# Kernel tuning notes

Hardware: AMD Instinct MI355X
Metric: run time of the kernel (lower is better)

Reference implementation:

```python
import jax, jax.numpy as jnp
import numpy as np

D = 64        # in_out_dim
M = 512       # hidden_dim
N = 4096      # batch
R = 10        # rank of quadratic term A (min(10, d+1))
ALPHA0 = 1.0  # alpha[0]
H = 1.0       # ResNet step h = 1/(nTh-1), nTh=2


def antideriv_tanh(x):
    # log(2*cosh(x)), numerically stable antiderivative of tanh
    ax = jnp.abs(x)
    return ax + jnp.log1p(jnp.exp(-2.0 * ax))


def setup_inputs() -> dict:
    key = jax.random.key(0)
    ks = jax.random.split(key, 10)
    f32 = jnp.float32
    return {
        "x":   jax.random.normal(ks[0], (N, D), f32),
        "t":   jax.random.uniform(ks[1], (), f32),
        "K0":  jax.random.normal(ks[2], (M, D + 1), f32) * (1.0 / np.sqrt(D + 1)),
        "b0":  jax.random.normal(ks[3], (M,), f32) * 0.1,
        "K1":  jax.random.normal(ks[4], (M, M), f32) * (1.0 / np.sqrt(M)),
        "b1":  jax.random.normal(ks[5], (M,), f32) * 0.1,
        "w":   jax.random.normal(ks[6], (M,), f32) * (1.0 / np.sqrt(M)),
        "A":   jax.random.normal(ks[7], (R, D + 1), f32) * (1.0 / np.sqrt(D + 1)),
        "c_w": jax.random.normal(ks[8], (D + 1,), f32) * 0.1,
        "c_b": jax.random.normal(ks[9], (), f32) * 0.1,
    }


def _tr_hess(s, K0, b0, K1, b1, w, A, c_w):
    # s: [N, d+1]; analytic gradient + Hessian trace of the OT-Flow potential.
    d = s.shape[1] - 1
    symA = A.T @ A                                   # [d+1, d+1]

    # forward through ResNet (nTh=2 -> one residual layer)
    opening = s @ K0.T + b0                          # [N, m]
    u0 = antideriv_tanh(opening)                     # [N, m]
    lin1 = u0 @ K1.T + b1                            # [N, m]

    tanh_open = jnp.tanh(opening)
    tanh_lin1 = jnp.tanh(lin1)

    # backward z-chain for the gradient
    z1 = w + H * (tanh_lin1 * w) @ K1                # [N, m]
    z0 = (tanh_open * z1) @ K0                       # [N, d+1]
    grad = z0 + s @ symA + c_w                       # [N, d+1]

    # trace of Hessian w.r.t. the first d coordinates
    Kopen = K0[:, :d]                                # [m, d]
    dt_open = 1.0 - tanh_open ** 2
    trH = (dt_open * z1) @ jnp.sum(Kopen ** 2, axis=1)          # [N]
    Jac = tanh_open[:, :, None] * Kopen[None]                    # [N, m, d]
    KJ = jnp.einsum('ij,njk->nik', K1, Jac)                      # [N, m, d]
    dt_lin1 = 1.0 - tanh_lin1 ** 2
    t1 = jnp.einsum('nj,njk->n', dt_lin1 * w, KJ ** 2)           # [N]
    trH = trH + H * t1 + jnp.trace(symA[:d, :d])
    return grad, trH


def reference(x, t, K0, b0, K1, b1, w, A, c_w, c_b):
    n = x.shape[0]
    s = jnp.concatenate([x, jnp.ones((n, 1), x.dtype) * t], axis=1)  # pad time
    gradPhi, trH = _tr_hess(s, K0, b0, K1, b1, w, A, c_w)
    dPhi_dx = gradPhi[:, :D]                         # [N, d]
    dPhi_dt = gradPhi[:, D:D + 1]                    # [N, 1]
    dz_dt = -(1.0 / ALPHA0) * dPhi_dx
    dlogp_dt = -(1.0 / ALPHA0) * trH[:, None]
    cost_L_dt = 0.5 * jnp.sum(dz_dt ** 2, axis=1, keepdims=True)
    cost_HJB_dt = jnp.abs(-dPhi_dt + ALPHA0 * cost_L_dt)
    return (dz_dt, dlogp_dt, cost_L_dt, cost_HJB_dt)
```

## Files before the change

### kernel.cpp

```cpp
#include <hip/hip_runtime.h>
#include <stdint.h>

#define D_  64
#define DP1 65
#define M_  512
#define N_  4096

typedef float f32x4 __attribute__((ext_vector_type(4)));
typedef _Float16 h8 __attribute__((ext_vector_type(8)));

__global__ void prep1(const float* __restrict__ A, const float* __restrict__ K0,
                      float* symA, float* sumK2, float* params){
  int t = threadIdx.x;
  for (int idx = t; idx < DP1*DP1; idx += 256){
    int e = idx / DP1, d = idx % DP1;
    float s = 0.f;
    for (int r = 0; r < 10; ++r) s += A[r*DP1+e]*A[r*DP1+d];
    symA[idx] = s;
  }
  for (int m = t; m < M_; m += 256){
    float s = 0.f;
    for (int k = 0; k < D_; ++k){ float v = K0[m*DP1+k]; s += v*v; }
    sumK2[m] = s;
  }
  __syncthreads();
  if (t == 0){
    float tr = 0.f;
    for (int d = 0; d < D_; ++d) tr += symA[d*DP1+d];
    params[0] = tr;
  }
}

__global__ void prep2(const float* __restrict__ K1, _Float16* K1h, _Float16* K1Th){
  __shared__ float tile[64][65];
  int r0 = blockIdx.x*64, c0 = blockIdx.y*64;
  int t = threadIdx.x;
  for (int it = 0; it < 16; ++it){
    int lin = it*256 + t;
    int r = lin >> 6, c = lin & 63;
    float v = K1[(r0+r)*M_ + c0+c];
    tile[r][c] = v;
    K1h[(r0+r)*M_ + c0+c] = (_Float16)v;
  }
  __syncthreads();
  for (int it = 0; it < 16; ++it){
    int lin = it*256 + t;
    int r = lin >> 6, c = lin & 63;
    K1Th[(c0+r)*M_ + (r0+c)] = (_Float16)tile[c][r];
  }
}

__global__ void prep3(const float* __restrict__ K0, _Float16* K0Th){
  int idx = blockIdx.x*256 + threadIdx.x;
  if (idx >= 80*M_) return;
  int d = idx / M_, i = idx % M_;
  float v = (d < DP1) ? K0[i*DP1 + d] : 0.f;
  K0Th[idx] = (_Float16)v;
}

__global__ void openk(const float* __restrict__ x, const float* __restrict__ tptr,
                      const float* __restrict__ K0, const float* __restrict__ b0,
                      _Float16* u0h, _Float16* ah,
                      float* trH0, const float* __restrict__ params){
  __shared__ float sS[64][66];
  __shared__ float sK[64][66];
  int n0 = blockIdx.x*64, m0 = blockIdx.y*64;
  int t = threadIdx.x;
  float tval = tptr[0];
  for (int it = 0; it < 17; ++it){
    int lin = it*256 + t;
    if (lin < 64*65){
      int r = lin/65, c = lin%65;
      sS[r][c] = (c < 64) ? x[(n0+r)*64 + c] : tval;
      sK[r][c] = K0[(m0+r)*DP1 + c];
    }
  }
  __syncthreads();
  int tn = (t>>4)*4, tm = (t&15)*4;
  float acc[4][4] = {};
  for (int e = 0; e < DP1; ++e){
    float sv[4], kv[4];
    for (int i=0;i<4;++i){ sv[i]=sS[tn+i][e]; kv[i]=sK[tm+i][e]; }
    for (int i=0;i<4;++i) for(int j=0;j<4;++j) acc[i][j] += sv[i]*kv[j];
  }
  for (int i=0;i<4;++i) for(int j=0;j<4;++j){
    int n = n0+tn+i, m = m0+tm+j;
    float o = acc[i][j] + b0[m];
    float a = tanhf(o);
    float ax = fabsf(o);
    float u0 = ax + log1pf(expf(-2.f*ax));
    u0h[n*M_+m] = (_Float16)u0;
    ah[n*M_+m]  = (_Float16)a;
  }
  if (m0 == 0 && t < 64) trH0[n0+t] = params[0];
}

template<int MODE>
__launch_bounds__(256, 4)
__global__ void gemm512(const _Float16* __restrict__ Ah, const _Float16* __restrict__ Wh,
                        const float* __restrict__ bias, const float* __restrict__ w,
                        const _Float16* __restrict__ ah, const float* __restrict__ sumK2,
                        _Float16* out0, _Float16* out1, float* trH0){
  int n0 = blockIdx.x*64, i0 = blockIdx.y*64;
  int t = threadIdx.x;
  int wv = t>>6, l = t&63;
  int r15 = l & 15;
  int krow = (l>>4)*8;
  const _Float16* abase = Ah + (size_t)(n0 + wv*16 + r15)*M_ + krow;
  const _Float16* wb0 = Wh + (size_t)(i0 +  0 + r15)*M_ + krow;
  const _Float16* wb1 = Wh + (size_t)(i0 + 16 + r15)*M_ + krow;
  const _Float16* wb2 = Wh + (size_t)(i0 + 32 + r15)*M_ + krow;
  const _Float16* wb3 = Wh + (size_t)(i0 + 48 + r15)*M_ + krow;
  f32x4 zero = {0.f,0.f,0.f,0.f};
  f32x4 acc[4]; for (int k=0;k<4;++k) acc[k]=zero;
  h8 af_c = *(const h8*)(abase);
  h8 bf_c0 = *(const h8*)(wb0);
  h8 bf_c1 = *(const h8*)(wb1);
  h8 bf_c2 = *(const h8*)(wb2);
  h8 bf_c3 = *(const h8*)(wb3);
  #pragma unroll
  for (int ii = 0; ii < 16; ++ii){
    const int j0 = ii*32;
    h8 af_n, bf_n0, bf_n1, bf_n2, bf_n3;
    if (ii < 15){
      af_n  = *(const h8*)(abase + j0 + 32);
      bf_n0 = *(const h8*)(wb0 + j0 + 32);
      bf_n1 = *(const h8*)(wb1 + j0 + 32);
      bf_n2 = *(const h8*)(wb2 + j0 + 32);
      bf_n3 = *(const h8*)(wb3 + j0 + 32);
    }
    acc[0] = __builtin_amdgcn_mfma_f32_16x16x32_f16(af_c, bf_c0, acc[0], 0, 0, 0);
    acc[1] = __builtin_amdgcn_mfma_f32_16x16x32_f16(af_c, bf_c1, acc[1], 0, 0, 0);
    acc[2] = __builtin_amdgcn_mfma_f32_16x16x32_f16(af_c, bf_c2, acc[2], 0, 0, 0);
    acc[3] = __builtin_amdgcn_mfma_f32_16x16x32_f16(af_c, bf_c3, acc[3], 0, 0, 0);
    if (ii < 15){
      af_c = af_n; bf_c0 = bf_n0; bf_c1 = bf_n1; bf_c2 = bf_n2; bf_c3 = bf_n3;
    }
  }
  if (MODE == 0){
    for (int kt=0;kt<4;++kt) for (int r=0;r<4;++r){
      int n = n0+wv*16+(l>>4)*4+r;
      int i = i0+kt*16+r15;
      float v = acc[kt][r] + bias[i];
      float tl = tanhf(v);
      out0[n*M_+i] = (_Float16)(tl*w[i]);
      out1[n*M_+i] = (_Float16)((1.f-tl*tl)*w[i]);
    }
  } else {
    for (int r=0;r<4;++r){
      int n = n0+wv*16+(l>>4)*4+r;
      float rowpart = 0.f;
      for (int kt=0;kt<4;++kt){
        int i = i0+kt*16+r15;
        float z1 = acc[kt][r] + w[i];
        float a = (float)ah[n*M_+i];
        out0[n*M_+i] = (_Float16)(a*z1);
        rowpart += (1.f-a*a)*z1*sumK2[i];
      }
      for (int m=1;m<16;m<<=1) rowpart += __shfl_xor(rowpart, m);
      if (r15==0) atomicAdd(&trH0[n], rowpart);
    }
  }
}

__launch_bounds__(256, 4)
__global__ void gemmz0(const _Float16* __restrict__ az1h, const _Float16* __restrict__ K0Th,
                       float* z0){
  int n0 = blockIdx.x*64;
  int t = threadIdx.x, wv = t>>6, l = t&63;
  int r15 = l & 15;
  int krow = (l>>4)*8;
  const _Float16* abase = az1h + (size_t)(n0 + wv*16 + r15)*M_ + krow;
  const _Float16* kb0 = K0Th + (size_t)( 0 + r15)*M_ + krow;
  const _Float16* kb1 = K0Th + (size_t)(16 + r15)*M_ + krow;
  const _Float16* kb2 = K0Th + (size_t)(32 + r15)*M_ + krow;
  const _Float16* kb3 = K0Th + (size_t)(48 + r15)*M_ + krow;
  const _Float16* kb4 = K0Th + (size_t)(64 + r15)*M_ + krow;
  f32x4 zero = {0.f,0.f,0.f,0.f};
  f32x4 acc[5]; for (int k=0;k<5;++k) acc[k]=zero;
  h8 af_c = *(const h8*)(abase);
  h8 b0c = *(const h8*)(kb0);
  h8 b1c = *(const h8*)(kb1);
  h8 b2c = *(const h8*)(kb2);
  h8 b3c = *(const h8*)(kb3);
  h8 b4c = *(const h8*)(kb4);
  #pragma unroll
  for (int ii = 0; ii < 16; ++ii){
    const int j0 = ii*32;
    h8 af_n, b0n, b1n, b2n, b3n, b4n;
    if (ii < 15){
      af_n = *(const h8*)(abase + j0 + 32);
      b0n = *(const h8*)(kb0 + j0 + 32);
      b1n = *(const h8*)(kb1 + j0 + 32);
      b2n = *(const h8*)(kb2 + j0 + 32);
      b3n = *(const h8*)(kb3 + j0 + 32);
      b4n = *(const h8*)(kb4 + j0 + 32);
    }
    acc[0] = __builtin_amdgcn_mfma_f32_16x16x32_f16(af_c, b0c, acc[0], 0, 0, 0);
    acc[1] = __builtin_amdgcn_mfma_f32_16x16x32_f16(af_c, b1c, acc[1], 0, 0, 0);
    acc[2] = __builtin_amdgcn_mfma_f32_16x16x32_f16(af_c, b2c, acc[2], 0, 0, 0);
    acc[3] = __builtin_amdgcn_mfma_f32_16x16x32_f16(af_c, b3c, acc[3], 0, 0, 0);
    acc[4] = __builtin_amdgcn_mfma_f32_16x16x32_f16(af_c, b4c, acc[4], 0, 0, 0);
    if (ii < 15){
      af_c = af_n; b0c = b0n; b1c = b1n; b2c = b2n; b3c = b3n; b4c = b4n;
    }
  }
  for (int dt=0; dt<5; ++dt) for (int r=0;r<4;++r){
    int n = n0+wv*16+(l>>4)*4+r;
    int d = dt*16+r15;
    z0[n*80+d] = acc[dt][r];
  }
}

__launch_bounds__(256, 2)
__global__ void kjk9(const _Float16* __restrict__ K1h, const _Float16* __restrict__ K0Th,
                     const _Float16* __restrict__ ah, const _Float16* __restrict__ ch,
                     float* trH0){
  __shared__ _Float16 sK1[64*512];
  __shared__ _Float16 sAv[8*512];
  int t = threadIdx.x;
  int n0 = blockIdx.x*8;
  int i0 = blockIdx.y*64;
  int wv = t>>6, l = t&63;
  int c15 = l & 15, g = l>>4;
  h8 kf[16];
  {
    const _Float16* kfp = K0Th + (size_t)(wv*16 + c15)*M_ + g*8;
    #pragma unroll
    for (int tt = 0; tt < 16; ++tt) kf[tt] = *(const h8*)(kfp + tt*32);
  }
  #pragma unroll
  for (int it = 0; it < 16; ++it){
    int cc = it*256 + t;
    int r = cc >> 6, c = cc & 63;
    h8 v = *(const h8*)(K1h + (size_t)(i0 + r)*M_ + c*8);
    *(h8*)(&sK1[r*512 + ((c ^ (r & 7))*8)]) = v;
  }
  #pragma unroll
  for (int it = 0; it < 2; ++it){
    int cc = it*256 + t;
    int s = cc >> 6, c = cc & 63;
    *(h8*)(&sAv[s*512 + c*8]) = *(const h8*)(ah + (size_t)(n0+s)*M_ + c*8);
  }
  __syncthreads();
  f32x4 zero = {0.f,0.f,0.f,0.f};
  f32x4 acc[4][8];
  #pragma unroll
  for (int tt=0;tt<4;++tt)
    #pragma unroll
    for (int s=0;s<8;++s) acc[tt][s]=zero;
  #pragma unroll
  for (int step = 0; step < 16; ++step){
    int p0 = (((step*4 + g) ^ (c15 & 7))*8);
    h8 bf0 = *(const h8*)(&sK1[(     c15)*512 + p0]);
    h8 bf1 = *(const h8*)(&sK1[(16 + c15)*512 + p0]);
    h8 bf2 = *(const h8*)(&sK1[(32 + c15)*512 + p0]);
    h8 bf3 = *(const h8*)(&sK1[(48 + c15)*512 + p0]);
    int aoff = step*32 + g*8;
    h8 k = kf[step];
    #pragma unroll
    for (int s = 0; s < 8; ++s){
      h8 av = *(const h8*)(&sAv[s*512 + aoff]);
      h8 ap = k*av;
      acc[0][s] = __builtin_amdgcn_mfma_f32_16x16x32_f16(ap, bf0, acc[0][s], 0, 0, 0);
      acc[1][s] = __builtin_amdgcn_mfma_f32_16x16x32_f16(ap, bf1, acc[1][s], 0, 0, 0);
      acc[2][s] = __builtin_amdgcn_mfma_f32_16x16x32_f16(ap, bf2, acc[2][s], 0, 0, 0);
      acc[3][s] = __builtin_amdgcn_mfma_f32_16x16x32_f16(ap, bf3, acc[3][s], 0, 0, 0);
    }
  }
  #pragma unroll
  for (int s = 0; s < 8; ++s){
    float part = 0.f;
    #pragma unroll
    for (int tt = 0; tt < 4; ++tt){
      float ci = (float)ch[(size_t)(n0+s)*M_ + i0 + tt*16 + c15];
      f32x4 a = acc[tt][s];
      part += ci*(a[0]*a[0] + a[1]*a[1] + a[2]*a[2] + a[3]*a[3]);
    }
    for (int m=32;m>=1;m>>=1) part += __shfl_xor(part, m);
    if (l == 0) atomicAdd(&trH0[n0+s], part);
  }
}

__global__ void finalk(const float* __restrict__ x, const float* __restrict__ tptr,
                       const float* __restrict__ symA, const float* __restrict__ c_w,
                       const float* __restrict__ z0, const float* __restrict__ trH0,
                       float* out){
  __shared__ float sA[DP1*DP1];
  int t = threadIdx.x;
  for (int i = t; i < DP1*DP1; i += 256) sA[i] = symA[i];
  __syncthreads();
  int wv = t>>6, l = t&63;
  int n = blockIdx.x*4 + wv;
  float tval = tptr[0];
  float sv = x[n*64 + l];
  float acc = z0[n*80 + l] + c_w[l];
  for (int e = 0; e < 64; ++e){
    float se = __shfl(sv, e);
    acc += se * sA[l*DP1 + e];
  }
  acc += tval * sA[l*DP1 + 64];
  float g64 = sv * sA[64*DP1 + l];
  for (int m=32;m>=1;m>>=1) g64 += __shfl_xor(g64, m);
  g64 += tval*sA[64*DP1+64] + z0[n*80+64] + c_w[64];
  float dz = -acc;
  out[n*64 + l] = dz;
  float q = dz*dz;
  for (int m=32;m>=1;m>>=1) q += __shfl_xor(q, m);
  float costL = 0.5f*q;
  if (l == 0){
    out[N_*64 + n]        = -trH0[n];
    out[N_*64 + N_ + n]   = costL;
    out[N_*64 + 2*N_ + n] = fabsf(-g64 + costL);
  }
}

extern "C" void kernel_launch(void* const* d_in, const int* in_sizes, int n_in,
                              void* d_out, int out_size, void* d_ws, size_t ws_size,
                              hipStream_t stream){
  const float* x   = (const float*)d_in[0];
  const float* tp  = (const float*)d_in[1];
  const float* K0  = (const float*)d_in[2];
  const float* b0  = (const float*)d_in[3];
  const float* K1  = (const float*)d_in[4];
  const float* b1  = (const float*)d_in[5];
  const float* w   = (const float*)d_in[6];
  const float* A   = (const float*)d_in[7];
  const float* c_w = (const float*)d_in[8];
  float* out = (float*)d_out;

  char* ws = (char*)d_ws;
  size_t off = 0;
  auto alloc = [&](size_t bytes)->void*{
    void* p = ws + off; off += bytes; off = (off + 255) & ~(size_t)255; return p;
  };
  _Float16* K1h   = (_Float16*)alloc(512*512*2);
  _Float16* K1Th  = (_Float16*)alloc(512*512*2);
  _Float16* K0Th  = (_Float16*)alloc(80*512*2);
  float* symA     = (float*)alloc(DP1*DP1*4);
  float* sumK2    = (float*)alloc(512*4);
  float* params   = (float*)alloc(256);
  _Float16* u0h   = (_Float16*)alloc((size_t)N_*M_*2);
  _Float16* ah    = (_Float16*)alloc((size_t)N_*M_*2);
  _Float16* tl1wh = (_Float16*)alloc((size_t)N_*M_*2);
  _Float16* ch    = (_Float16*)alloc((size_t)N_*M_*2);
  _Float16* az1h  = (_Float16*)alloc((size_t)N_*M_*2);
  float* z0       = (float*)alloc((size_t)N_*80*4);
  float* trH0     = (float*)alloc(N_*4);

  prep1<<<1, 256, 0, stream>>>(A, K0, symA, sumK2, params);
  prep2<<<dim3(8,8), 256, 0, stream>>>(K1, K1h, K1Th);
  prep3<<<160, 256, 0, stream>>>(K0, K0Th);
  openk<<<dim3(N_/64, M_/64), 256, 0, stream>>>(x, tp, K0, b0, u0h, ah, trH0, params);
  gemm512<0><<<dim3(N_/64, M_/64), 256, 0, stream>>>(u0h, K1h, b1, w, nullptr, nullptr,
                                                     tl1wh, ch, nullptr);
  gemm512<1><<<dim3(N_/64, M_/64), 256, 0, stream>>>(tl1wh, K1Th, nullptr, w, ah, sumK2,
                                                     az1h, nullptr, trH0);
  gemmz0<<<N_/64, 256, 0, stream>>>(az1h, K0Th, z0);
  kjk9<<<dim3(N_/8, 8), 256, 0, stream>>>(K1h, K0Th, ah, ch, trH0);
  finalk<<<N_/4, 256, 0, stream>>>(x, tp, symA, c_w, z0, trH0, out);
}
```

Measured before the change: 235.2 us.

## Merge prep and opening kernels, load K1 tile via global_load_lds in kjk

Four small preprocessing kernels and the opening-layer kernel are merged into a single launch whose block index selects the role. This removes three launch boundaries and serialization gaps. The symA trace term moves into the final kernel as a wave reduction, so trH0 is simply zeroed. In the Hessian-trace kernel, the K1 tile is staged into LDS with direct global-to-LDS loads, and the activation rows are read straight from global memory instead of through LDS, trading LDS traffic for repeated global/L1 loads.

```diff
diff --git a/kernel.cpp b/kernel.cpp
--- a/kernel.cpp
+++ b/kernel.cpp
@@ -9,90 +9,84 @@
 typedef float f32x4 __attribute__((ext_vector_type(4)));
 typedef _Float16 h8 __attribute__((ext_vector_type(8)));
 
-__global__ void prep1(const float* __restrict__ A, const float* __restrict__ K0,
-                      float* symA, float* sumK2, float* params){
+__global__ void prepk(const float* __restrict__ A, const float* __restrict__ K0,
+                      const float* __restrict__ K1, const float* __restrict__ x,
+                      const float* __restrict__ tptr, const float* __restrict__ b0,
+                      float* symA, float* sumK2,
+                      _Float16* K1h, _Float16* K1Th, _Float16* K0Th,
+                      _Float16* u0h, _Float16* ah, float* trH0){
+  __shared__ float shm[2*64*66];
+  int b = blockIdx.x;
   int t = threadIdx.x;
-  for (int idx = t; idx < DP1*DP1; idx += 256){
-    int e = idx / DP1, d = idx % DP1;
-    float s = 0.f;
-    for (int r = 0; r < 10; ++r) s += A[r*DP1+e]*A[r*DP1+d];
-    symA[idx] = s;
-  }
-  for (int m = t; m < M_; m += 256){
-    float s = 0.f;
-    for (int k = 0; k < D_; ++k){ float v = K0[m*DP1+k]; s += v*v; }
-    sumK2[m] = s;
-  }
-  __syncthreads();
-  if (t == 0){
-    float tr = 0.f;
-    for (int d = 0; d < D_; ++d) tr += symA[d*DP1+d];
-    params[0] = tr;
-  }
-}
-
-__global__ void prep2(const float* __restrict__ K1, _Float16* K1h, _Float16* K1Th){
-  __shared__ float tile[64][65];
-  int r0 = blockIdx.x*64, c0 = blockIdx.y*64;
-  int t = threadIdx.x;
-  for (int it = 0; it < 16; ++it){
-    int lin = it*256 + t;
-    int r = lin >> 6, c = lin & 63;
-    float v = K1[(r0+r)*M_ + c0+c];
-    tile[r][c] = v;
-    K1h[(r0+r)*M_ + c0+c] = (_Float16)v;
-  }
-  __syncthreads();
-  for (int it = 0; it < 16; ++it){
-    int lin = it*256 + t;
-    int r = lin >> 6, c = lin & 63;
-    K1Th[(c0+r)*M_ + (r0+c)] = (_Float16)tile[c][r];
-  }
-}
-
-__global__ void prep3(const float* __restrict__ K0, _Float16* K0Th){
-  int idx = blockIdx.x*256 + threadIdx.x;
-  if (idx >= 80*M_) return;
-  int d = idx / M_, i = idx % M_;
-  float v = (d < DP1) ? K0[i*DP1 + d] : 0.f;
-  K0Th[idx] = (_Float16)v;
-}
-
-__global__ void openk(const float* __restrict__ x, const float* __restrict__ tptr,
-                      const float* __restrict__ K0, const float* __restrict__ b0,
-                      _Float16* u0h, _Float16* ah,
-                      float* trH0, const float* __restrict__ params){
-  __shared__ float sS[64][66];
-  __shared__ float sK[64][66];
-  int n0 = blockIdx.x*64, m0 = blockIdx.y*64;
-  int t = threadIdx.x;
-  float tval = tptr[0];
-  for (int it = 0; it < 17; ++it){
-    int lin = it*256 + t;
-    if (lin < 64*65){
-      int r = lin/65, c = lin%65;
-      sS[r][c] = (c < 64) ? x[(n0+r)*64 + c] : tval;
-      sK[r][c] = K0[(m0+r)*DP1 + c];
-    }
-  }
-  __syncthreads();
-  int tn = (t>>4)*4, tm = (t&15)*4;
-  float acc[4][4] = {};
-  for (int e = 0; e < DP1; ++e){
-    float sv[4], kv[4];
-    for (int i=0;i<4;++i){ sv[i]=sS[tn+i][e]; kv[i]=sK[tm+i][e]; }
-    for (int i=0;i<4;++i) for(int j=0;j<4;++j) acc[i][j] += sv[i]*kv[j];
-  }
-  for (int i=0;i<4;++i) for(int j=0;j<4;++j){
-    int n = n0+tn+i, m = m0+tm+j;
-    float o = acc[i][j] + b0[m];
-    float a = tanhf(o);
-    float ax = fabsf(o);
-    float u0 = ax + log1pf(expf(-2.f*ax));
-    u0h[n*M_+m] = (_Float16)u0;
-    ah[n*M_+m]  = (_Float16)a;
-  }
-  if (m0 == 0 && t < 64) trH0[n0+t] = params[0];
+  if (b == 0){
+    for (int idx = t; idx < DP1*DP1; idx += 256){
+      int e = idx / DP1, d = idx % DP1;
+      float s = 0.f;
+      for (int r = 0; r < 10; ++r) s += A[r*DP1+e]*A[r*DP1+d];
+      symA[idx] = s;
+    }
+    for (int m = t; m < M_; m += 256){
+      float s = 0.f;
+      for (int k = 0; k < D_; ++k){ float v = K0[m*DP1+k]; s += v*v; }
+      sumK2[m] = s;
+    }
+  } else if (b < 65){
+    int bb = b - 1;
+    int r0 = (bb>>3)*64, c0 = (bb&7)*64;
+    float* tile = shm;
+    for (int it = 0; it < 16; ++it){
+      int lin = it*256 + t;
+      int r = lin >> 6, c = lin & 63;
+      float v = K1[(r0+r)*M_ + c0+c];
+      tile[r*65+c] = v;
+      K1h[(r0+r)*M_ + c0+c] = (_Float16)v;
+    }
+    __syncthreads();
+    for (int it = 0; it < 16; ++it){
+      int lin = it*256 + t;
+      int r = lin >> 6, c = lin & 63;
+      K1Th[(c0+r)*M_ + (r0+c)] = (_Float16)tile[c*65+r];
+    }
+  } else if (b < 225){
+    int idx = (b-65)*256 + t;
+    if (idx < 80*M_){
+      int d = idx / M_, i = idx % M_;
+      float v = (d < DP1) ? K0[i*DP1 + d] : 0.f;
+      K0Th[idx] = (_Float16)v;
+    }
+  } else {
+    int bb = b - 225;
+    int n0 = (bb & 63)*64, m0 = (bb >> 6)*64;
+    float* sS = shm;
+    float* sK = shm + 64*66;
+    float tval = tptr[0];
+    for (int it = 0; it < 17; ++it){
+      int lin = it*256 + t;
+      if (lin < 64*65){
+        int r = lin/65, c = lin%65;
+        sS[r*66+c] = (c < 64) ? x[(n0+r)*64 + c] : tval;
+        sK[r*66+c] = K0[(m0+r)*DP1 + c];
+      }
+    }
+    __syncthreads();
+    int tn = (t>>4)*4, tm = (t&15)*4;
+    float acc[4][4] = {};
+    for (int e = 0; e < DP1; ++e){
+      float sv[4], kv[4];
+      for (int i=0;i<4;++i){ sv[i]=sS[(tn+i)*66+e]; kv[i]=sK[(tm+i)*66+e]; }
+      for (int i=0;i<4;++i) for(int j=0;j<4;++j) acc[i][j] += sv[i]*kv[j];
+    }
+    for (int i=0;i<4;++i) for(int j=0;j<4;++j){
+      int n = n0+tn+i, m = m0+tm+j;
+      float o = acc[i][j] + b0[m];
+      float a = tanhf(o);
+      float ax = fabsf(o);
+      float u0 = ax + log1pf(expf(-2.f*ax));
+      u0h[n*M_+m] = (_Float16)u0;
+      ah[n*M_+m]  = (_Float16)a;
+    }
+    if (m0 == 0 && t < 64) trH0[n0+t] = 0.f;
+  }
 }
 
 template<int MODE>
@@ -213,11 +207,10 @@
 }
 
 __launch_bounds__(256, 2)
-__global__ void kjk9(const _Float16* __restrict__ K1h, const _Float16* __restrict__ K0Th,
-                     const _Float16* __restrict__ ah, const _Float16* __restrict__ ch,
-                     float* trH0){
+__global__ void kjk10(const _Float16* __restrict__ K1h, const _Float16* __restrict__ K0Th,
+                      const _Float16* __restrict__ ah, const _Float16* __restrict__ ch,
+                      float* trH0){
   __shared__ _Float16 sK1[64*512];
-  __shared__ _Float16 sAv[8*512];
   int t = threadIdx.x;
   int n0 = blockIdx.x*8;
   int i0 = blockIdx.y*64;
@@ -231,16 +224,11 @@
   }
   #pragma unroll
   for (int it = 0; it < 16; ++it){
-    int cc = it*256 + t;
-    int r = cc >> 6, c = cc & 63;
-    h8 v = *(const h8*)(K1h + (size_t)(i0 + r)*M_ + c*8);
-    *(h8*)(&sK1[r*512 + ((c ^ (r & 7))*8)]) = v;
-  }
-  #pragma unroll
-  for (int it = 0; it < 2; ++it){
-    int cc = it*256 + t;
-    int s = cc >> 6, c = cc & 63;
-    *(h8*)(&sAv[s*512 + c*8]) = *(const h8*)(ah + (size_t)(n0+s)*M_ + c*8);
+    int r = it*4 + wv;
+    const _Float16* src = K1h + (size_t)(i0 + r)*M_ + ((l ^ (r & 7))*8);
+    __builtin_amdgcn_global_load_lds(
+        (const __attribute__((address_space(1))) void*)src,
+        (__attribute__((address_space(3))) void*)(&sK1[r*512]), 16, 0, 0);
   }
   __syncthreads();
   f32x4 zero = {0.f,0.f,0.f,0.f};
@@ -249,6 +237,7 @@
   for (int tt=0;tt<4;++tt)
     #pragma unroll
     for (int s=0;s<8;++s) acc[tt][s]=zero;
+  const _Float16* ab = ah + (size_t)n0*M_ + g*8;
   #pragma unroll
   for (int step = 0; step < 16; ++step){
     int p0 = (((step*4 + g) ^ (c15 & 7))*8);
@@ -256,11 +245,10 @@
     h8 bf1 = *(const h8*)(&sK1[(16 + c15)*512 + p0]);
     h8 bf2 = *(const h8*)(&sK1[(32 + c15)*512 + p0]);
     h8 bf3 = *(const h8*)(&sK1[(48 + c15)*512 + p0]);
-    int aoff = step*32 + g*8;
     h8 k = kf[step];
     #pragma unroll
     for (int s = 0; s < 8; ++s){
-      h8 av = *(const h8*)(&sAv[s*512 + aoff]);
+      h8 av = *(const h8*)(ab + (size_t)s*M_ + step*32);
       h8 ap = k*av;
       acc[0][s] = __builtin_amdgcn_mfma_f32_16x16x32_f16(ap, bf0, acc[0][s], 0, 0, 0);
       acc[1][s] = __builtin_amdgcn_mfma_f32_16x16x32_f16(ap, bf1, acc[1][s], 0, 0, 0);
@@ -300,6 +288,8 @@
     acc += se * sA[l*DP1 + e];
   }
   acc += tval * sA[l*DP1 + 64];
+  float trd = sA[l*66];
+  for (int m=32;m>=1;m>>=1) trd += __shfl_xor(trd, m);
   float g64 = sv * sA[64*DP1 + l];
   for (int m=32;m>=1;m>>=1) g64 += __shfl_xor(g64, m);
   g64 += tval*sA[64*DP1+64] + z0[n*80+64] + c_w[64];
@@ -309,7 +299,7 @@
   for (int m=32;m>=1;m>>=1) q += __shfl_xor(q, m);
   float costL = 0.5f*q;
   if (l == 0){
-    out[N_*64 + n]        = -trH0[n];
+    out[N_*64 + n]        = -(trH0[n] + trd);
     out[N_*64 + N_ + n]   = costL;
     out[N_*64 + 2*N_ + n] = fabsf(-g64 + costL);
   }
@@ -339,7 +329,6 @@
   _Float16* K0Th  = (_Float16*)alloc(80*512*2);
   float* symA     = (float*)alloc(DP1*DP1*4);
   float* sumK2    = (float*)alloc(512*4);
-  float* params   = (float*)alloc(256);
   _Float16* u0h   = (_Float16*)alloc((size_t)N_*M_*2);
   _Float16* ah    = (_Float16*)alloc((size_t)N_*M_*2);
   _Float16* tl1wh = (_Float16*)alloc((size_t)N_*M_*2);
@@ -348,15 +337,13 @@
   float* z0       = (float*)alloc((size_t)N_*80*4);
   float* trH0     = (float*)alloc(N_*4);
 
-  prep1<<<1, 256, 0, stream>>>(A, K0, symA, sumK2, params);
-  prep2<<<dim3(8,8), 256, 0, stream>>>(K1, K1h, K1Th);
-  prep3<<<160, 256, 0, stream>>>(K0, K0Th);
-  openk<<<dim3(N_/64, M_/64), 256, 0, stream>>>(x, tp, K0, b0, u0h, ah, trH0, params);
+  prepk<<<737, 256, 0, stream>>>(A, K0, K1, x, tp, b0, symA, sumK2,
+                                 K1h, K1Th, K0Th, u0h, ah, trH0);
   gemm512<0><<<dim3(N_/64, M_/64), 256, 0, stream>>>(u0h, K1h, b1, w, nullptr, nullptr,
                                                      tl1wh, ch, nullptr);
   gemm512<1><<<dim3(N_/64, M_/64), 256, 0, stream>>>(tl1wh, K1Th, nullptr, w, ah, sumK2,
                                                      az1h, nullptr, trH0);
   gemmz0<<<N_/64, 256, 0, stream>>>(az1h, K0Th, z0);
-  kjk9<<<dim3(N_/8, 8), 256, 0, stream>>>(K1h, K0Th, ah, ch, trH0);
+  kjk10<<<dim3(N_/8, 8), 256, 0, stream>>>(K1h, K0Th, ah, ch, trH0);
   finalk<<<N_/4, 256, 0, stream>>>(x, tp, symA, c_w, z0, trH0, out);
 }
```

After: 254.6 us. 8.2% more time.
